# Kernel optimization log

Hardware: AMD Instinct MI355X
Metric: run time of the kernel (lower is better)

Reference implementation:

```python
import jax, jax.numpy as jnp
import numpy as np

N, E, B = 51200, 819200, 64
F, G, GH, LH, LOUT = 64, 64, 128, 128, 1


def setup_inputs() -> dict:
    key = jax.random.key(0)
    ks = jax.random.split(key, 10)
    x = jax.random.normal(ks[0], (N, F), dtype=jnp.float32)
    e = jax.random.uniform(ks[1], (N, 1), dtype=jnp.float32)  # data.p[:, 0].view(-1, 1)
    edge_index = jax.random.randint(ks[2], (2, E), 0, N, dtype=jnp.int64)
    batch = jnp.sort(jax.random.randint(ks[3], (N,), 0, B, dtype=jnp.int64))

    def init_w(k, fan_in, fan_out):
        return (jax.random.normal(k, (fan_in, fan_out), dtype=jnp.float32)
                / np.float32(np.sqrt(fan_in)))

    # global PTConv nn: MLP(2F -> GH -> G)
    gW1 = init_w(ks[4], 2 * F, GH)
    gb1 = jnp.zeros((GH,), dtype=jnp.float32)
    gW2 = init_w(ks[5], GH, G)
    gb2 = jnp.zeros((G,), dtype=jnp.float32)
    # local PTConv nn: MLP(2*(F+G) -> LH -> 1)
    lW1 = init_w(ks[6], 2 * (F + G), LH)
    lb1 = jnp.zeros((LH,), dtype=jnp.float32)
    lW2 = init_w(ks[7], LH, LOUT)
    lb2 = jnp.zeros((LOUT,), dtype=jnp.float32)
    return {"x": x, "e": e, "edge_index": edge_index, "batch": batch,
            "gW1": gW1, "gb1": gb1, "gW2": gW2, "gb2": gb2,
            "lW1": lW1, "lb1": lb1, "lW2": lW2, "lb2": lb2}


def _mlp(h, W1, b1, W2, b2):
    return jax.nn.relu(h @ W1 + b1) @ W2 + b2


def _ptconv(x, edge_index, W1, b1, W2, b2, num_nodes):
    # PyG convention: edge_index[0]=src (j), edge_index[1]=dst (i); aggr='add'
    src, dst = edge_index[0], edge_index[1]
    h = jnp.concatenate([x[dst], x[src]], axis=-1)  # [E, 2*Fin] edge gather
    m = _mlp(h, W1, b1, W2, b2)                      # [E, Fout] edge MLP
    return jax.ops.segment_sum(m, dst, num_segments=num_nodes)  # scatter-add


def reference(x, e, edge_index, batch,
              gW1, gb1, gW2, gb2, lW1, lb1, lW2, lb2):
    n = x.shape[0]
    # EFNGlobal: PTConv -> energy weighting -> global_add_pool
    g = _ptconv(x, edge_index, gW1, gb1, gW2, gb2, n)   # [N, G]
    g = e * g                                           # e = p[:, 0:1]
    pooled = jax.ops.segment_sum(g, batch, num_segments=B)  # [B, G]
    # EFNLocal: broadcast per-graph scalars to nodes, concat, PTConv
    scalars = pooled[batch]                             # [N, G]
    xl = jnp.concatenate([x, scalars], axis=-1)         # [N, F+G]
    w_i = _ptconv(xl, edge_index, lW1, lb1, lW2, lb2, n)  # [N, 1]
    return w_i
```

## Files before the change

kernel.cpp:

```cpp
#include <hip/hip_runtime.h>
#include <hip/hip_bf16.h>

#define NN 51200
#define EE 819200
#define BB 64
#define NS 32
#define NPWG 8
#define NPWL 4
#define NBUCK 512
#define NPB 100
#define CAP 4096

typedef __attribute__((ext_vector_type(8))) short short8;
typedef __attribute__((ext_vector_type(4))) float f32x4;

__device__ __forceinline__ ushort f2bf(float f) {
    unsigned int u = __float_as_uint(f);
    unsigned int r = (u + 0x7FFFu + ((u >> 16) & 1u)) >> 16;
    return (ushort)r;
}
__device__ __forceinline__ unsigned int cvt_pk_bf16(float lo, float hi) {
    unsigned int r;
    asm("v_cvt_pk_bf16_f32 %0, %1, %2" : "=v"(r) : "v"(lo), "v"(hi));
    return r;
}

__global__ void prep_weights(const float* __restrict__ gW1, const float* __restrict__ lW1,
                             ushort* __restrict__ W1p, ushort* __restrict__ L1p) {
    int tid = threadIdx.x;
    for (int idx = tid; idx < 64 * 256; idx += 512) {
        int i = idx & 7, c = (idx >> 3) & 255, q = idx >> 11;
        int k = (q >> 2) * 32 + (q & 3) * 8 + i;
        W1p[idx] = f2bf(c < 128 ? gW1[k * 128 + c] : gW1[(64 + k) * 128 + (c - 128)]);
        L1p[idx] = f2bf(c < 128 ? lW1[k * 128 + c] : lW1[(128 + k) * 128 + (c - 128)]);
    }
}

__global__ void bucketA_kernel(const int* __restrict__ eidx, int* __restrict__ bcnt,
                               int2* __restrict__ btmp) {
    int i = blockIdx.x * 256 + threadIdx.x;
    int d = eidx[EE + i], s = eidx[i];
    int bkt = d / NPB;
    int pos = atomicAdd(&bcnt[bkt * 16], 1);
    btmp[(long)bkt * CAP + pos] = make_int2(s, d);
}

__global__ __launch_bounds__(512) void bucket_scan_kernel(const int* __restrict__ bcnt,
                                                          int* __restrict__ bbase) {
    __shared__ int s[NBUCK];
    const int t = threadIdx.x;
    int v = bcnt[t * 16];
    s[t] = v;
    __syncthreads();
    for (int o = 1; o < NBUCK; o <<= 1) {
        int u = (t >= o) ? s[t - o] : 0;
        __syncthreads();
        s[t] += u;
        __syncthreads();
    }
    bbase[t] = s[t] - v;
}

__global__ __launch_bounds__(256) void bucketB_kernel(const int2* __restrict__ btmp,
                                                      const int* __restrict__ bcnt,
                                                      const int* __restrict__ bbase,
                                                      int* __restrict__ offs,
                                                      int* __restrict__ csr) {
    __shared__ int lcnt[NPB];
    __shared__ int lofs[NPB];
    __shared__ int lcur[NPB];
    __shared__ int2 pairs[2048];
    const int bkt = blockIdx.x, tid = threadIdx.x;
    const int cnt = bcnt[bkt * 16];
    const int base = bbase[bkt];
    for (int j = tid; j < NPB; j += 256) lcnt[j] = 0;
    __syncthreads();
    for (int i = tid; i < cnt; i += 256) {
        int2 p = btmp[(long)bkt * CAP + i];
        if (i < 2048) pairs[i] = p;
        atomicAdd(&lcnt[p.y - bkt * NPB], 1);
    }
    __syncthreads();
    if (tid == 0) {
        int run = base;
        for (int j = 0; j < NPB; ++j) { lofs[j] = run; run += lcnt[j]; }
    }
    __syncthreads();
    for (int j = tid; j < NPB; j += 256) {
        lcur[j] = lofs[j];
        offs[bkt * NPB + j] = lofs[j];
    }
    if (bkt == NBUCK - 1 && tid == 0) offs[NN] = EE;
    __syncthreads();
    for (int i = tid; i < cnt; i += 256) {
        int2 p = (i < 2048) ? pairs[i] : btmp[(long)bkt * CAP + i];
        int pos = atomicAdd(&lcur[p.y - bkt * NPB], 1);
        csr[pos] = p.x;
    }
}

__global__ __launch_bounds__(512) void pq_gemm(
        const float* __restrict__ x, const ushort* __restrict__ Wp,
        const float* __restrict__ bias1, const float* __restrict__ T12,
        const int* __restrict__ batch, ushort* __restrict__ out) {
    const int tid = threadIdx.x;
    const int w = tid >> 6, l = tid & 63, lr = l & 15, lg = l >> 4;
    const int node = blockIdx.x * 128 + w * 16 + lr;

    short8 xa[2];
#pragma unroll
    for (int ks = 0; ks < 2; ++ks) {
        const float4* bp = reinterpret_cast<const float4*>(x + (long)node * 64 + ks * 32 + lg * 8);
        float4 f0 = bp[0], f1 = bp[1];
        union { short8 s; unsigned int u[4]; } t;
        t.u[0] = cvt_pk_bf16(f0.x, f0.y);
        t.u[1] = cvt_pk_bf16(f0.z, f0.w);
        t.u[2] = cvt_pk_bf16(f1.x, f1.y);
        t.u[3] = cvt_pk_bf16(f1.z, f1.w);
        xa[ks] = t.s;
    }
    f32x4 acc[16];
#pragma unroll
    for (int t = 0; t < 16; ++t)
#pragma unroll
        for (int i = 0; i < 4; ++i)
            acc[t][i] = (t < 8) ? bias1[t * 16 + lg * 4 + i] : 0.f;
#pragma unroll
    for (int ks = 0; ks < 2; ++ks)
#pragma unroll
        for (int t = 0; t < 16; ++t) {
            short8 wf = *reinterpret_cast<const short8*>(Wp + (((ks * 4 + lg) * 256) + t * 16 + lr) * 8);
            acc[t] = __builtin_amdgcn_mfma_f32_16x16x32_bf16(wf, xa[ks], acc[t], 0, 0, 0);
        }
    if (T12) {
        const float* tp = T12 + (long)batch[node] * 256;
#pragma unroll
        for (int t = 0; t < 16; ++t)
#pragma unroll
            for (int i = 0; i < 4; ++i)
                acc[t][i] += tp[t * 16 + lg * 4 + i];
    }
#pragma unroll
    for (int t = 0; t < 16; ++t) {
        uint2 v;
        v.x = cvt_pk_bf16(acc[t][0], acc[t][1]);
        v.y = cvt_pk_bf16(acc[t][2], acc[t][3]);
        *reinterpret_cast<uint2*>(out + (long)node * 256 + t * 16 + lg * 4) = v;
    }
}

__global__ __launch_bounds__(256) void global_edge(
        const ushort* __restrict__ PQ, const int* __restrict__ csr,
        const int* __restrict__ offs, const float* __restrict__ e,
        const int* __restrict__ batch,
        float* __restrict__ hidpart, float* __restrict__ esumpart) {
    const int tid = threadIdx.x;
    const int w = tid >> 6, l = tid & 63;
    const int wid = blockIdx.x * 4 + w;
    const int node0 = __builtin_amdgcn_readfirstlane(wid * NPWG);
    const int slot = wid & (NS - 1);

    float accp0 = 0.f, accp1 = 0.f, eacc = 0.f;
    int curb = batch[node0];

    for (int n = 0; n < NPWG; ++n) {
        const int node = node0 + n;
        const int off  = offs[node];
        const int cnt  = offs[node + 1] - off;
        const int bb   = batch[node];
        const float ev = e[node];
        if (bb != curb) {
            float* hp = hidpart + (long)slot * (BB * 128) + curb * 128;
            atomicAdd(hp + 2 * l, accp0);
            atomicAdd(hp + 2 * l + 1, accp1);
            if (l == 0) atomicAdd(&esumpart[slot * BB + curb], eacc);
            accp0 = accp1 = eacc = 0.f;
            curb = bb;
        }
        if (cnt <= 0) continue;
        const unsigned int pdu = *reinterpret_cast<const unsigned int*>(PQ + (long)node * 256 + 2 * l);
        const float p0 = __uint_as_float(pdu << 16);
        const float p1 = __uint_as_float(pdu & 0xFFFF0000u);
        float h0 = 0.f, h1 = 0.f;
        int g = 0;
        for (; g + 8 <= cnt; g += 8) {
            unsigned int qv[8];
#pragma unroll
            for (int k = 0; k < 8; ++k) {
                const int s = csr[off + g + k];
                qv[k] = *reinterpret_cast<const unsigned int*>(PQ + (long)s * 256 + 128 + 2 * l);
            }
#pragma unroll
            for (int k = 0; k < 8; ++k) {
                h0 += fmaxf(p0 + __uint_as_float(qv[k] << 16), 0.f);
                h1 += fmaxf(p1 + __uint_as_float(qv[k] & 0xFFFF0000u), 0.f);
            }
        }
        for (; g < cnt; ++g) {
            const int s = csr[off + g];
            const unsigned int qv = *reinterpret_cast<const unsigned int*>(PQ + (long)s * 256 + 128 + 2 * l);
            h0 += fmaxf(p0 + __uint_as_float(qv << 16), 0.f);
            h1 += fmaxf(p1 + __uint_as_float(qv & 0xFFFF0000u), 0.f);
        }
        accp0 += ev * h0; accp1 += ev * h1; eacc += ev * (float)cnt;
    }
    {
        float* hp = hidpart + (long)slot * (BB * 128) + curb * 128;
        atomicAdd(hp + 2 * l, accp0);
        atomicAdd(hp + 2 * l + 1, accp1);
        if (l == 0) atomicAdd(&esumpart[slot * BB + curb], eacc);
    }
}

__global__ __launch_bounds__(256) void pooled_t12_kernel(
        const float* __restrict__ hidpart, const float* __restrict__ esumpart,
        const float* __restrict__ gW2, const float* __restrict__ gb2,
        const float* __restrict__ lW1, float* __restrict__ T12) {
    __shared__ float hs[128];
    __shared__ float qacc[4][64];
    __shared__ float pb[64];
    __shared__ float esv;
    const int b = blockIdx.x, tid = threadIdx.x;
    if (tid < 128) {
        float s = 0.f;
        for (int sl = 0; sl < NS; ++sl) s += hidpart[(long)sl * (BB * 128) + b * 128 + tid];
        hs[tid] = s;
    } else if (tid == 128) {
        float s = 0.f;
        for (int sl = 0; sl < NS; ++sl) s += esumpart[sl * BB + b];
        esv = s;
    }
    __syncthreads();
    {
        int col = tid & 63, qr = tid >> 6;
        float a = 0.f;
        for (int k = qr * 32; k < qr * 32 + 32; ++k) a += hs[k] * gW2[k * 64 + col];
        qacc[qr][col] = a;
    }
    __syncthreads();
    if (tid < 64) pb[tid] = qacc[0][tid] + qacc[1][tid] + qacc[2][tid] + qacc[3][tid] + esv * gb2[tid];
    __syncthreads();
    const float* col = (tid < 128) ? (lW1 + 64 * 128 + tid) : (lW1 + 192 * 128 + (tid - 128));
    float acc = 0.f;
    for (int k = 0; k < 64; ++k) acc += pb[k] * col[k * 128];
    T12[b * 256 + tid] = acc;
}

__global__ __launch_bounds__(256) void local_edge(
        const ushort* __restrict__ PQL, const int* __restrict__ csr,
        const int* __restrict__ offs, const float* __restrict__ lW2,
        const float* __restrict__ lb2, float* __restrict__ out) {
    const int tid = threadIdx.x;
    const int w = tid >> 6, l = tid & 63;
    const int wid = blockIdx.x * 4 + w;
    const int node0 = __builtin_amdgcn_readfirstlane(wid * NPWL);
    const float w20 = lW2[2 * l], w21 = lW2[2 * l + 1];
    const float b2v = lb2[0];

    for (int n = 0; n < NPWL; ++n) {
        const int node = node0 + n;
        const int off = offs[node];
        const int cnt = offs[node + 1] - off;
        float dacc = 0.f;
        if (cnt > 0) {
            const unsigned int pdu = *reinterpret_cast<const unsigned int*>(PQL + (long)node * 256 + 2 * l);
            const float p0 = __uint_as_float(pdu << 16);
            const float p1 = __uint_as_float(pdu & 0xFFFF0000u);
            int g = 0;
            for (; g + 8 <= cnt; g += 8) {
                unsigned int qv[8];
#pragma unroll
                for (int k = 0; k < 8; ++k) {
                    const int s = csr[off + g + k];
                    qv[k] = *reinterpret_cast<const unsigned int*>(PQL + (long)s * 256 + 128 + 2 * l);
                }
#pragma unroll
                for (int k = 0; k < 8; ++k) {
                    dacc += fmaxf(p0 + __uint_as_float(qv[k] << 16), 0.f) * w20
                          + fmaxf(p1 + __uint_as_float(qv[k] & 0xFFFF0000u), 0.f) * w21;
                }
            }
            for (; g < cnt; ++g) {
                const int s = csr[off + g];
                const unsigned int qv = *reinterpret_cast<const unsigned int*>(PQL + (long)s * 256 + 128 + 2 * l);
                dacc += fmaxf(p0 + __uint_as_float(qv << 16), 0.f) * w20
                      + fmaxf(p1 + __uint_as_float(qv & 0xFFFF0000u), 0.f) * w21;
            }
            dacc += __shfl_xor(dacc, 1, 64);
            dacc += __shfl_xor(dacc, 2, 64);
            dacc += __shfl_xor(dacc, 4, 64);
            dacc += __shfl_xor(dacc, 8, 64);
            dacc += __shfl_xor(dacc, 16, 64);
            dacc += __shfl_xor(dacc, 32, 64);
        }
        if (l == 0) out[node] = dacc + (float)cnt * b2v;
    }
}

extern "C" void kernel_launch(void* const* d_in, const int* in_sizes, int n_in,
                              void* d_out, int out_size, void* d_ws, size_t ws_size,
                              hipStream_t stream) {
    const float* x   = (const float*)d_in[0];
    const float* e   = (const float*)d_in[1];
    const int*   ei  = (const int*)d_in[2];
    const int*   bat = (const int*)d_in[3];
    const float* gW1 = (const float*)d_in[4];
    const float* gb1 = (const float*)d_in[5];
    const float* gW2 = (const float*)d_in[6];
    const float* gb2 = (const float*)d_in[7];
    const float* lW1 = (const float*)d_in[8];
    const float* lb1 = (const float*)d_in[9];
    const float* lW2 = (const float*)d_in[10];
    const float* lb2 = (const float*)d_in[11];

    char* ws = (char*)d_ws;
    ushort* W1p     = (ushort*)(ws);
    ushort* L1p     = (ushort*)(ws + 32768);
    float*  T12     = (float*)(ws + 65536);
    float*  esumpart= (float*)(ws + 131072);
    float*  hidpart = (float*)(ws + 139264);
    int*    offs    = (int*)(ws + 1187840);
    int*    bcnt    = (int*)(ws + 1392672);
    int*    bbase   = (int*)(ws + 1425440);
    int*    csr     = (int*)(ws + 1427488);
    ushort* PQ      = (ushort*)(ws + 4704288);
    int2*   btmp    = (int2*)PQ;

    hipMemsetAsync(bcnt, 0, 32768, stream);
    hipMemsetAsync(esumpart, 0, 8192 + 1048576, stream);
    hipMemsetAsync(d_out, 0, (size_t)out_size * sizeof(float), stream);

    prep_weights<<<1, 512, 0, stream>>>(gW1, lW1, W1p, L1p);
    bucketA_kernel<<<EE / 256, 256, 0, stream>>>(ei, bcnt, btmp);
    bucket_scan_kernel<<<1, NBUCK, 0, stream>>>(bcnt, bbase);
    bucketB_kernel<<<NBUCK, 256, 0, stream>>>(btmp, bcnt, bbase, offs, csr);

    pq_gemm<<<NN / 128, 512, 0, stream>>>(x, W1p, gb1, nullptr, bat, PQ);
    global_edge<<<NN / (4 * NPWG), 256, 0, stream>>>(PQ, csr, offs, e, bat, hidpart, esumpart);
    pooled_t12_kernel<<<BB, 256, 0, stream>>>(hidpart, esumpart, gW2, gb2, lW1, T12);
    pq_gemm<<<NN / 128, 512, 0, stream>>>(x, L1p, lb1, T12, bat, PQ);
    local_edge<<<NN / (4 * NPWL), 256, 0, stream>>>(PQ, csr, offs, lW2, lb2, (float*)d_out);
}
```

Before: 201.5 us.

## Block-local shared-memory bucketing of edges and deeper gather unroll

The edge bucketing kernel now loads 4096 edges per block into shared memory, counts and prefix-scans the buckets locally, reserves one global slot range per bucket with a single atomic, then writes the edges grouped by bucket. This replaces one global atomic per edge with one per bucket per block and makes the writes contiguous. Separately, the global and local edge gather loops gain a 16-wide unrolled stage so more loads are in flight, at the cost of extra registers. Each block thread walks its bucket's edges serially, so the write phase may be unbalanced across threads.

```diff
diff --git a/kernel.cpp b/kernel.cpp
--- a/kernel.cpp
+++ b/kernel.cpp
@@ -10,6 +10,7 @@
 #define NBUCK 512
 #define NPB 100
 #define CAP 4096
+#define EPB 4096
 
 typedef __attribute__((ext_vector_type(8))) short short8;
 typedef __attribute__((ext_vector_type(4))) float f32x4;
@@ -36,13 +37,54 @@
     }
 }
 
-__global__ void bucketA_kernel(const int* __restrict__ eidx, int* __restrict__ bcnt,
-                               int2* __restrict__ btmp) {
-    int i = blockIdx.x * 256 + threadIdx.x;
-    int d = eidx[EE + i], s = eidx[i];
-    int bkt = d / NPB;
-    int pos = atomicAdd(&bcnt[bkt * 16], 1);
-    btmp[(long)bkt * CAP + pos] = make_int2(s, d);
+__global__ __launch_bounds__(512) void bucketA_kernel(const int* __restrict__ eidx,
+                                                      int* __restrict__ bcnt,
+                                                      int2* __restrict__ btmp) {
+    __shared__ int2 sp[EPB];
+    __shared__ ushort sb[EPB];
+    __shared__ ushort perm[EPB];
+    __shared__ int cnts[NBUCK];
+    __shared__ int lofs[NBUCK];
+    __shared__ int lcur[NBUCK];
+    __shared__ int gbase[NBUCK];
+    const int tid = threadIdx.x;
+    const int base = blockIdx.x * EPB;
+
+    cnts[tid] = 0;
+    __syncthreads();
+    for (int i = tid; i < EPB; i += 512) {
+        int d = eidx[EE + base + i], s = eidx[base + i];
+        sp[i] = make_int2(s, d);
+        int b = d / NPB;
+        sb[i] = (ushort)b;
+        atomicAdd(&cnts[b], 1);
+    }
+    __syncthreads();
+    const int v = cnts[tid];
+    lofs[tid] = v;
+    __syncthreads();
+    for (int o = 1; o < NBUCK; o <<= 1) {
+        int u = (tid >= o) ? lofs[tid - o] : 0;
+        __syncthreads();
+        lofs[tid] += u;
+        __syncthreads();
+    }
+    const int excl = lofs[tid] - v;
+    lofs[tid] = excl;
+    lcur[tid] = excl;
+    gbase[tid] = (v > 0) ? atomicAdd(&bcnt[tid * 16], v) : 0;
+    __syncthreads();
+    for (int i = tid; i < EPB; i += 512) {
+        int pos = atomicAdd(&lcur[sb[i]], 1);
+        perm[pos] = (ushort)i;
+    }
+    __syncthreads();
+    {
+        const int c = cnts[tid];
+        const int lo = lofs[tid];
+        int2* dst = btmp + (long)tid * CAP + gbase[tid];
+        for (int j = 0; j < c; ++j) dst[j] = sp[perm[lo + j]];
+    }
 }
 
 __global__ __launch_bounds__(512) void bucket_scan_kernel(const int* __restrict__ bcnt,
@@ -183,6 +225,19 @@
         const float p1 = __uint_as_float(pdu & 0xFFFF0000u);
         float h0 = 0.f, h1 = 0.f;
         int g = 0;
+        for (; g + 16 <= cnt; g += 16) {
+            unsigned int qv[16];
+#pragma unroll
+            for (int k = 0; k < 16; ++k) {
+                const int s = csr[off + g + k];
+                qv[k] = *reinterpret_cast<const unsigned int*>(PQ + (long)s * 256 + 128 + 2 * l);
+            }
+#pragma unroll
+            for (int k = 0; k < 16; ++k) {
+                h0 += fmaxf(p0 + __uint_as_float(qv[k] << 16), 0.f);
+                h1 += fmaxf(p1 + __uint_as_float(qv[k] & 0xFFFF0000u), 0.f);
+            }
+        }
         for (; g + 8 <= cnt; g += 8) {
             unsigned int qv[8];
 #pragma unroll
@@ -267,6 +322,19 @@
             const float p0 = __uint_as_float(pdu << 16);
             const float p1 = __uint_as_float(pdu & 0xFFFF0000u);
             int g = 0;
+            for (; g + 16 <= cnt; g += 16) {
+                unsigned int qv[16];
+#pragma unroll
+                for (int k = 0; k < 16; ++k) {
+                    const int s = csr[off + g + k];
+                    qv[k] = *reinterpret_cast<const unsigned int*>(PQL + (long)s * 256 + 128 + 2 * l);
+                }
+#pragma unroll
+                for (int k = 0; k < 16; ++k) {
+                    dacc += fmaxf(p0 + __uint_as_float(qv[k] << 16), 0.f) * w20
+                          + fmaxf(p1 + __uint_as_float(qv[k] & 0xFFFF0000u), 0.f) * w21;
+                }
+            }
             for (; g + 8 <= cnt; g += 8) {
                 unsigned int qv[8];
 #pragma unroll
@@ -331,7 +399,7 @@
     hipMemsetAsync(d_out, 0, (size_t)out_size * sizeof(float), stream);
 
     prep_weights<<<1, 512, 0, stream>>>(gW1, lW1, W1p, L1p);
-    bucketA_kernel<<<EE / 256, 256, 0, stream>>>(ei, bcnt, btmp);
+    bucketA_kernel<<<EE / EPB, 512, 0, stream>>>(ei, bcnt, btmp);
     bucket_scan_kernel<<<1, NBUCK, 0, stream>>>(bcnt, bbase);
     bucketB_kernel<<<NBUCK, 256, 0, stream>>>(btmp, bcnt, bbase, offs, csr);
 
```

After: 190.3 us. -5.6%, faster.
